# Optimization experiments

Hardware: AMD Instinct MI355X
Metric: run time of the kernel (lower is better)

The kernel has to match this reference:

```python
import jax, jax.numpy as jnp
import numpy as np

COLOR_SIZE = 4
SIZE = 64
FILTERS = 512
LENGTH = SIZE * SIZE * 3  # 12288


def setup_inputs() -> dict:
    key = jax.random.key(0)
    k1, k2, k3 = jax.random.split(key, 3)
    example = jax.random.randint(k1, (8, SIZE, SIZE, 3), 0, COLOR_SIZE, dtype=jnp.int32)
    kernel = jax.random.normal(k2, (FILTERS, LENGTH), dtype=jnp.float32)
    bias = jnp.zeros((FILTERS,), dtype=jnp.float32)
    dense_w = jax.random.normal(k3, (FILTERS, COLOR_SIZE), dtype=jnp.float32) * 0.02
    dense_b = jnp.zeros((COLOR_SIZE,), dtype=jnp.float32)
    return {"example": example, "kernel": kernel, "bias": bias,
            "dense_w": dense_w, "dense_b": dense_b}


def reference(example, kernel, bias, dense_w, dense_b):
    B = example.shape[0]
    L = kernel.shape[1]  # 12288
    # normalize int pixels to [-1, 1)
    x = example.astype(jnp.float32) / COLOR_SIZE * 2.0 - 1.0
    x = x.reshape(B, L)                                   # [B, L]
    # FFT-based long (causal full) convolution, fft_length = 2L
    Xf = jnp.fft.rfft(x, n=2 * L, axis=-1)                # [B, L+1] complex64
    Kf = jnp.fft.rfft(kernel, n=2 * L, axis=-1)           # [F, L+1]
    y = jnp.fft.irfft(Xf[:, None, :] * Kf[None, :, :], n=2 * L, axis=-1)[..., :L]  # [B, F, L]
    y = jnp.transpose(y, (0, 2, 1)) + bias                # [B, L, F]
    y = jax.nn.relu(y)
    out = y @ dense_w + dense_b                           # [B, L, color_size]
    return out.reshape(B, SIZE, SIZE, 3, COLOR_SIZE).astype(jnp.float32)
```

## Files before the change

### kernel.cpp

```cpp
#include <hip/hip_runtime.h>

#define FF 512
#define LL 12288
#define NJC 1560
#define NR 128

typedef _Float16 half8  __attribute__((ext_vector_type(8)));
typedef float    f32x16 __attribute__((ext_vector_type(16)));

__global__ __launch_bounds__(256) void build_At(const float* __restrict__ kern,
                                                _Float16* __restrict__ At) {
    int tid  = blockIdx.x * 256 + threadIdx.x;
    int lane = tid & 63;
    int rest = tid >> 6;
    int kc   = rest % 768;
    int ft   = rest / 768;
    int f    = ft * 32 + (lane & 31);
    int d0   = kc * 16 + (lane >> 5) * 8;
    const float* src = kern + (size_t)f * LL + d0;
    half8 v;
#pragma unroll
    for (int i = 0; i < 8; ++i) v[i] = (_Float16)src[i];
    ((half8*)At)[tid] = v;
}

__global__ __launch_bounds__(256) void build_XB(const int* __restrict__ ex,
                                                _Float16* __restrict__ XB) {
    int tid = blockIdx.x * 256 + threadIdx.x;
    int r  = tid & 127;
    int jc = tid >> 7;
    int s  = r >> 3, b = r & 7;
    int j0 = jc * 8;
    half8 v;
#pragma unroll
    for (int i = 0; i < 8; ++i) {
        int idx = LL - 1 - (j0 + i) - s;
        float x = 0.f;
        if (idx >= 0) x = (float)ex[b * LL + idx] * 0.5f - 1.0f;
        v[i] = (_Float16)x;
    }
    ((half8*)XB)[tid] = v;
}

__global__ __launch_bounds__(256) void init_out(const float* __restrict__ db,
                                                float* __restrict__ out) {
    int tid = blockIdx.x * 256 + threadIdx.x;
    out[tid] = db[tid & 3];
}

__device__ __forceinline__ void gl_lds16(const half8* g, half8* l) {
    __builtin_amdgcn_global_load_lds((const __attribute__((address_space(1))) void*)g,
                                     (__attribute__((address_space(3))) void*)l, 16, 0, 0);
}

__global__ __launch_bounds__(256, 2) void conv_main(const _Float16* __restrict__ At,
                                                    const _Float16* __restrict__ XB,
                                                    const float* __restrict__ bias,
                                                    const float* __restrict__ dw,
                                                    float* __restrict__ out) {
    __shared__ half8 Abuf[2][8][4][64];

    int bx    = blockIdx.x;
    int slot  = bx & 7;
    int f_blk = slot >> 1;
    int n_blk = 383 - ((bx >> 3) * 2 + (slot & 1));
    int n0 = n_blk << 5;
    int S  = n_blk + 1;
    int M  = (S + 3) >> 2;

    int tid  = threadIdx.x;
    int lane = tid & 63;
    int wid  = tid >> 6;
    int kh   = lane >> 5;
    int bb   = lane & 7;
    int nh   = (lane >> 3) & 3;

    const half8* Ag = (const half8*)At;
    const half8* ag = Ag + ((size_t)(f_blk * 4 + wid) * 768) * 64 + lane;

    const half8* Bg = (const half8*)XB;
    const half8* pB[2];
#pragma unroll
    for (int ti = 0; ti < 2; ++ti) {
        int n_base = n0 + (wid * 2 + ti) * 4;
        int Qt = LL - 1 - n_base - nh;
        int s  = Qt & 7;
        int jc0 = Qt >> 3;
        pB[ti] = Bg + (size_t)(jc0 + kh) * 128 + s * 8 + bb;
    }

    f32x16 acc[4][2];
#pragma unroll
    for (int mt = 0; mt < 4; ++mt)
#pragma unroll
        for (int ti = 0; ti < 2; ++ti)
#pragma unroll
            for (int r = 0; r < 16; ++r) acc[mt][ti][r] = 0.f;

#pragma unroll
    for (int kc = 0; kc < 8; ++kc)
        gl_lds16(ag + (size_t)kc * 64, &Abuf[0][kc][wid][lane]);
    half8 bf[2][2][2];
#pragma unroll
    for (int ti = 0; ti < 2; ++ti) {
        bf[0][0][ti] = pB[ti][0];
        bf[0][1][ti] = pB[ti][256];
        bf[1][0][ti] = pB[ti][512];
        bf[1][1][ti] = pB[ti][768];
    }
    __syncthreads();

    for (int mc = 0; mc < M; ++mc) {
        int buf = mc & 1;
        if (mc + 1 < M) {
            size_t oa = (size_t)(mc + 1) * 512;
#pragma unroll
            for (int kc = 0; kc < 8; ++kc)
                gl_lds16(ag + oa + (size_t)kc * 64, &Abuf[buf ^ 1][kc][wid][lane]);
        }
#pragma unroll
        for (int d4 = 0; d4 < 4; ++d4) {
            int dcg = mc * 4 + d4;
            int p   = d4 & 1;
            half8 a0[4], a1[4];
#pragma unroll
            for (int mt = 0; mt < 4; ++mt) {
                a0[mt] = Abuf[buf][d4 * 2][mt][lane];
                a1[mt] = Abuf[buf][d4 * 2 + 1][mt][lane];
            }
#pragma unroll
            for (int mt = 0; mt < 4; ++mt)
#pragma unroll
                for (int ti = 0; ti < 2; ++ti)
                    acc[mt][ti] = __builtin_amdgcn_mfma_f32_32x32x16_f16(a0[mt], bf[p][0][ti], acc[mt][ti], 0, 0, 0);
#pragma unroll
            for (int mt = 0; mt < 4; ++mt)
#pragma unroll
                for (int ti = 0; ti < 2; ++ti)
                    acc[mt][ti] = __builtin_amdgcn_mfma_f32_32x32x16_f16(a1[mt], bf[p][1][ti], acc[mt][ti], 0, 0, 0);
            size_t ob = (size_t)(dcg + 2) * 512;
#pragma unroll
            for (int ti = 0; ti < 2; ++ti) {
                bf[p][0][ti] = pB[ti][ob];
                bf[p][1][ti] = pB[ti][ob + 256];
            }
        }
        __syncthreads();
    }

    float p[2][4] = {{0.f}};
#pragma unroll
    for (int mt = 0; mt < 4; ++mt) {
#pragma unroll
        for (int reg = 0; reg < 16; ++reg) {
            int row = (reg & 3) + 8 * (reg >> 2) + 4 * kh;
            int f   = f_blk * 128 + mt * 32 + row;
            float bs = bias[f];
            float4 w = *(const float4*)(dw + (size_t)f * 4);
#pragma unroll
            for (int ti = 0; ti < 2; ++ti) {
                float y = fmaxf(acc[mt][ti][reg] + bs, 0.f);
                p[ti][0] += y * w.x; p[ti][1] += y * w.y;
                p[ti][2] += y * w.z; p[ti][3] += y * w.w;
            }
        }
    }
#pragma unroll
    for (int ti = 0; ti < 2; ++ti)
#pragma unroll
        for (int c = 0; c < 4; ++c) {
            float v = p[ti][c];
            v += __shfl_xor(v, 32, 64);
            p[ti][c] = v;
        }
    if (kh == 0) {
#pragma unroll
        for (int ti = 0; ti < 2; ++ti) {
            int n = n0 + (wid * 2 + ti) * 4 + nh;
            float* o = out + ((size_t)bb * LL + n) * 4;
#pragma unroll
            for (int c = 0; c < 4; ++c) atomicAdd(o + c, p[ti][c]);
        }
    }
}

extern "C" void kernel_launch(void* const* d_in, const int* in_sizes, int n_in,
                              void* d_out, int out_size, void* d_ws, size_t ws_size,
                              hipStream_t stream) {
    const int*   ex   = (const int*)d_in[0];
    const float* kern = (const float*)d_in[1];
    const float* bias = (const float*)d_in[2];
    const float* dw   = (const float*)d_in[3];
    const float* db   = (const float*)d_in[4];
    float* out = (float*)d_out;

    _Float16* At = (_Float16*)d_ws;
    _Float16* XB = (_Float16*)((char*)d_ws + (size_t)FF * LL * 2);

    hipLaunchKernelGGL(build_At, dim3(3072), dim3(256), 0, stream, kern, At);
    hipLaunchKernelGGL(build_XB, dim3(780),  dim3(256), 0, stream, ex, XB);
    hipLaunchKernelGGL(init_out, dim3(1536), dim3(256), 0, stream, db, out);
    hipLaunchKernelGGL(conv_main, dim3(1536), dim3(256), 0, stream, At, XB, bias, dw, out);
}
```

Baseline: 546.8 us.

## Stage Toeplitz B operand through shared LDS ring buffer, halve A stage depth

Each wave previously read its B (shifted input) fragments straight from global memory into registers. Now the block cooperatively loads contiguous XB chunks into a 32-entry LDS ring with async global-to-LDS loads, and every wave reads its shifted fragments from that ring. The A double-buffer stage also shrinks from 8 to 4 k-chunks per iteration, which doubles the iteration count and the number of barriers. The aim is to cut redundant global traffic for the heavily overlapping B windows, at the cost of extra LDS reads, possible bank conflicts and more frequent synchronization.

Measured after the change: 567.4 us. 1.04x slower.

```diff
diff --git a/kernel.cpp b/kernel.cpp
--- a/kernel.cpp
+++ b/kernel.cpp
@@ -58,7 +58,8 @@
                                                     const float* __restrict__ bias,
                                                     const float* __restrict__ dw,
                                                     float* __restrict__ out) {
-    __shared__ half8 Abuf[2][8][4][64];
+    __shared__ half8 Abuf[2][4][4][64];
+    __shared__ half8 Bring[32][64];
 
     int bx    = blockIdx.x;
     int slot  = bx & 7;
@@ -66,7 +67,9 @@
     int n_blk = 383 - ((bx >> 3) * 2 + (slot & 1));
     int n0 = n_blk << 5;
     int S  = n_blk + 1;
-    int M  = (S + 3) >> 2;
+    int M  = (S + 1) >> 1;
+    int Q0 = LL - 1 - n0;
+    int J0 = (Q0 - 28) >> 3;
 
     int tid  = threadIdx.x;
     int lane = tid & 63;
@@ -76,17 +79,15 @@
     int nh   = (lane >> 3) & 3;
 
     const half8* Ag = (const half8*)At;
-    const half8* ag = Ag + ((size_t)(f_blk * 4 + wid) * 768) * 64 + lane;
-
     const half8* Bg = (const half8*)XB;
-    const half8* pB[2];
+
+    int c0[2], rowi[2];
 #pragma unroll
     for (int ti = 0; ti < 2; ++ti) {
-        int n_base = n0 + (wid * 2 + ti) * 4;
-        int Qt = LL - 1 - n_base - nh;
-        int s  = Qt & 7;
-        int jc0 = Qt >> 3;
-        pB[ti] = Bg + (size_t)(jc0 + kh) * 128 + s * 8 + bb;
+        int T  = wid * 2 + ti;
+        int QT = Q0 - 4 * T;
+        c0[ti]   = (QT >> 3) + kh;
+        rowi[ti] = ((QT & 7) - nh) * 8 + bb;
     }
 
     f32x16 acc[4][2];
@@ -98,52 +99,51 @@
             for (int r = 0; r < 16; ++r) acc[mt][ti][r] = 0.f;
 
 #pragma unroll
-    for (int kc = 0; kc < 8; ++kc)
-        gl_lds16(ag + (size_t)kc * 64, &Abuf[0][kc][wid][lane]);
-    half8 bf[2][2][2];
-#pragma unroll
-    for (int ti = 0; ti < 2; ++ti) {
-        bf[0][0][ti] = pB[ti][0];
-        bf[0][1][ti] = pB[ti][256];
-        bf[1][0][ti] = pB[ti][512];
-        bf[1][1][ti] = pB[ti][768];
+    for (int i = 0; i < 4; ++i)
+        gl_lds16(Ag + ((size_t)(f_blk * 4 + wid) * 768 + i) * 64 + lane,
+                 &Abuf[0][i][wid][lane]);
+    for (int c = wid; c < 18; c += 4) {
+        int jc = J0 + c;
+        gl_lds16(Bg + (size_t)jc * 128 + lane, &Bring[jc & 31][lane]);
     }
     __syncthreads();
 
     for (int mc = 0; mc < M; ++mc) {
         int buf = mc & 1;
         if (mc + 1 < M) {
-            size_t oa = (size_t)(mc + 1) * 512;
-#pragma unroll
-            for (int kc = 0; kc < 8; ++kc)
-                gl_lds16(ag + oa + (size_t)kc * 64, &Abuf[buf ^ 1][kc][wid][lane]);
-        }
-#pragma unroll
-        for (int d4 = 0; d4 < 4; ++d4) {
-            int dcg = mc * 4 + d4;
-            int p   = d4 & 1;
-            half8 a0[4], a1[4];
-#pragma unroll
-            for (int mt = 0; mt < 4; ++mt) {
-                a0[mt] = Abuf[buf][d4 * 2][mt][lane];
-                a1[mt] = Abuf[buf][d4 * 2 + 1][mt][lane];
+#pragma unroll
+            for (int i = 0; i < 4; ++i) {
+                int kc = (mc + 1) * 4 + i;
+                gl_lds16(Ag + ((size_t)(f_blk * 4 + wid) * 768 + kc) * 64 + lane,
+                         &Abuf[buf ^ 1][i][wid][lane]);
             }
-#pragma unroll
-            for (int mt = 0; mt < 4; ++mt)
+        }
+        {
+            int cb = J0 + 18 + 8 * mc + wid * 2;
+            gl_lds16(Bg + (size_t)cb * 128 + lane, &Bring[cb & 31][lane]);
+            gl_lds16(Bg + (size_t)(cb + 1) * 128 + lane, &Bring[(cb + 1) & 31][lane]);
+        }
+#pragma unroll
+        for (int sub = 0; sub < 2; ++sub) {
+            int dc = mc * 2 + sub;
+            half8 af[2][4], bfr[2][2];
+#pragma unroll
+            for (int h = 0; h < 2; ++h)
+#pragma unroll
+                for (int mt = 0; mt < 4; ++mt)
+                    af[h][mt] = Abuf[buf][sub * 2 + h][mt][lane];
+#pragma unroll
+            for (int h = 0; h < 2; ++h)
 #pragma unroll
                 for (int ti = 0; ti < 2; ++ti)
-                    acc[mt][ti] = __builtin_amdgcn_mfma_f32_32x32x16_f16(a0[mt], bf[p][0][ti], acc[mt][ti], 0, 0, 0);
-#pragma unroll
-            for (int mt = 0; mt < 4; ++mt)
-#pragma unroll
-                for (int ti = 0; ti < 2; ++ti)
-                    acc[mt][ti] = __builtin_amdgcn_mfma_f32_32x32x16_f16(a1[mt], bf[p][1][ti], acc[mt][ti], 0, 0, 0);
-            size_t ob = (size_t)(dcg + 2) * 512;
-#pragma unroll
-            for (int ti = 0; ti < 2; ++ti) {
-                bf[p][0][ti] = pB[ti][ob];
-                bf[p][1][ti] = pB[ti][ob + 256];
-            }
+                    bfr[h][ti] = Bring[(c0[ti] + 4 * dc + 2 * h) & 31][rowi[ti]];
+#pragma unroll
+            for (int h = 0; h < 2; ++h)
+#pragma unroll
+                for (int mt = 0; mt < 4; ++mt)
+#pragma unroll
+                    for (int ti = 0; ti < 2; ++ti)
+                        acc[mt][ti] = __builtin_amdgcn_mfma_f32_32x32x16_f16(af[h][mt], bfr[h][ti], acc[mt][ti], 0, 0, 0);
         }
         __syncthreads();
     }
```
